# Optimization experiments

Measured on AMD Instinct MI355X. Metric: run time of the kernel, lower is better.

## Reference

```python
import jax, jax.numpy as jnp
import numpy as np


def _ccl(x, w, b):
    # FFT-domain circular conv: rfft2 -> complex multiply + sum over c_in -> irfft2 + bias
    H, W = x.shape[-2], x.shape[-1]
    xf = jnp.fft.rfft2(x)                 # [B, Ci, H, Wf] complex
    wf = jnp.fft.rfft2(w, s=(H, W))       # [Co, Ci, H, Wf] complex
    hf = jnp.einsum('bihw,oihw->bohw', xf, wf)
    return jnp.fft.irfft2(hf, s=(H, W)) + b[:, None, None]


def _maxpool(x, ph, pw):
    B, C, H, W = x.shape
    return x.reshape(B, C, H // ph, ph, W // pw, pw).max(axis=(3, 5))


def _upsample_zero(x, sh, sw):
    B, C, H, W = x.shape
    y = jnp.zeros((B, C, H * sh, W * sw), dtype=x.dtype)
    return y.at[:, :, ::sh, ::sw].set(x)


def setup_inputs() -> dict:
    key = jax.random.key(0)
    ks = jax.random.split(key, 11)
    inp = {"x": jax.random.normal(ks[0], (16, 2, 64, 256), dtype=jnp.float32)}
    specs = [  # (c_out, c_in, kh, kw)
        (50, 1, 3, 7), (50, 50, 3, 7), (50, 50, 3, 5), (50, 50, 3, 7), (1, 50, 3, 7)]
    for i, (co, ci, kh, kw) in enumerate(specs):
        K = float(np.sqrt(1.0 / (ci * kh * kw)))
        inp[f"w{i+1}"] = (2 * jax.random.uniform(ks[2 * i + 1], (co, ci, kh, kw), dtype=jnp.float32) - 1) * K
        inp[f"b{i+1}"] = (2 * jax.random.uniform(ks[2 * i + 2], (co,), dtype=jnp.float32) - 1) * K
    return inp


def reference(x, w1, b1, w2, b2, w3, b3, w4, b4, w5, b5):
    H, W = x.shape[-2], x.shape[-1]
    h = x.reshape(-1, 1, H, W)                       # [2B, 1, 64, 256]
    h = jax.nn.relu(_maxpool(_ccl(h, w1, b1), 2, 4))  # [2B, 50, 32, 64]
    h = jax.nn.relu(_maxpool(_ccl(h, w2, b2), 2, 4))  # [2B, 50, 16, 16]
    h = h.reshape(-1, 2, h.shape[-3], h.shape[-2], h.shape[-1])
    h = h[:, 0] + h[:, 1].mean(axis=(-1, -2))[..., None, None]  # [B, 50, 16, 16]
    h = jax.nn.relu(_ccl(_upsample_zero(h, 2, 4), w3, b3))       # [B, 50, 32, 64]
    h = jax.nn.relu(_ccl(_upsample_zero(h, 2, 4), w4, b4))       # [B, 50, 64, 256]
    h = jax.nn.sigmoid(_ccl(h, w5, b5))                          # [B, 1, 64, 256]
    return h.squeeze(1)
```

## Files before the change

### kernel.cpp

```cpp
#include <hip/hip_runtime.h>
#include <math.h>

__global__ void kprep(const float* __restrict__ w2, const float* __restrict__ w3,
                      const float* __restrict__ w4, float* __restrict__ w2t,
                      float* __restrict__ w3t, float* __restrict__ w4t) {
  int i = blockIdx.x * 256 + threadIdx.x;
  if (i < 52500) {
    int co = i % 50, r = i / 50;
    w2t[i] = w2[co * 1050 + r];
    w4t[i] = w4[co * 1050 + r];
  } else {
    int j = i - 52500;
    if (j < 37500) {
      int co = j % 50, r = j / 50;
      w3t[j] = w3[co * 750 + r];
    }
  }
}

__global__ __launch_bounds__(256) void k1(const float* __restrict__ x,
                                          const float* __restrict__ w1,
                                          const float* __restrict__ b1,
                                          float* __restrict__ a1) {
  int b = blockIdx.z;
  int pr0 = blockIdx.x * 4;
  int co0 = blockIdx.y * 10;
  int ty = threadIdx.x >> 6;
  int pc = threadIdx.x & 63;
  int pr = pr0 + ty;
  const float* xb = x + b * (64 * 256);
  float xw[4][10];
#pragma unroll
  for (int r = 0; r < 4; ++r) {
    int row = (2 * pr - 2 + r) & 63;
#pragma unroll
    for (int c = 0; c < 10; ++c) {
      int col = (4 * pc - 6 + c) & 255;
      xw[r][c] = xb[row * 256 + col];
    }
  }
#pragma unroll
  for (int cq = 0; cq < 10; ++cq) {
    int co = co0 + cq;
    const float* wp = w1 + co * 21;
    float m = -1e30f;
#pragma unroll
    for (int iy = 0; iy < 2; ++iy) {
#pragma unroll
      for (int jx = 0; jx < 4; ++jx) {
        float s = 0.f;
#pragma unroll
        for (int di = 0; di < 3; ++di)
#pragma unroll
          for (int dj = 0; dj < 7; ++dj)
            s = fmaf(xw[iy + 2 - di][jx + 6 - dj], wp[di * 7 + dj], s);
        m = fmaxf(m, s);
      }
    }
    float v = fmaxf(m + b1[co], 0.f);
    a1[((b * 50 + co) * 32 + pr) * 64 + pc] = v;
  }
}

__global__ __launch_bounds__(256) void k2(const float* __restrict__ a1,
                                          const float* __restrict__ w2t,
                                          const float* __restrict__ b2,
                                          float* __restrict__ a2) {
  __shared__ __align__(16) float sm[3840];
  int b = blockIdx.z;
  int r0 = blockIdx.x * 4;
  int co0 = blockIdx.y * 10;
  int y = threadIdx.x >> 6;
  int xcol = threadIdx.x & 63;
  const float* p[7];
#pragma unroll
  for (int dj = 0; dj < 7; ++dj) p[dj] = sm + y * 64 + ((xcol - dj) & 63);
  float acc[10];
#pragma unroll
  for (int co = 0; co < 10; ++co) acc[co] = b2[co0 + co];
  const float* ain = a1 + b * (50 * 2048);
  for (int cci = 0; cci < 5; ++cci) {
    __syncthreads();
    for (int e = threadIdx.x; e < 960; e += 256) {
      int ci = e / 96;
      int rem = e - ci * 96;
      int rr = rem >> 4;
      int c4 = rem & 15;
      int row = (r0 - 2 + rr) & 31;
      *(float4*)&sm[(ci * 6 + rr) * 64 + c4 * 4] =
          *(const float4*)&ain[(cci * 10 + ci) * 2048 + row * 64 + c4 * 4];
    }
    __syncthreads();
    const float* q0 = p[0]; const float* q1 = p[1]; const float* q2 = p[2];
    const float* q3 = p[3]; const float* q4 = p[4]; const float* q5 = p[5];
    const float* q6 = p[6];
    for (int ci = 0; ci < 10; ++ci) {
      const float* wci = w2t + (cci * 10 + ci) * 1050 + co0;
#pragma unroll
      for (int di = 0; di < 3; ++di) {
        const int ro = (2 - di) * 64;
        float xv0 = q0[ro], xv1 = q1[ro], xv2 = q2[ro], xv3 = q3[ro];
        float xv4 = q4[ro], xv5 = q5[ro], xv6 = q6[ro];
        const float* wr = wci + di * 7 * 50;
#pragma unroll
        for (int co = 0; co < 10; ++co) acc[co] = fmaf(xv0, wr[co], acc[co]);
#pragma unroll
        for (int co = 0; co < 10; ++co) acc[co] = fmaf(xv1, wr[50 + co], acc[co]);
#pragma unroll
        for (int co = 0; co < 10; ++co) acc[co] = fmaf(xv2, wr[100 + co], acc[co]);
#pragma unroll
        for (int co = 0; co < 10; ++co) acc[co] = fmaf(xv3, wr[150 + co], acc[co]);
#pragma unroll
        for (int co = 0; co < 10; ++co) acc[co] = fmaf(xv4, wr[200 + co], acc[co]);
#pragma unroll
        for (int co = 0; co < 10; ++co) acc[co] = fmaf(xv5, wr[250 + co], acc[co]);
#pragma unroll
        for (int co = 0; co < 10; ++co) acc[co] = fmaf(xv6, wr[300 + co], acc[co]);
      }
      q0 += 384; q1 += 384; q2 += 384; q3 += 384; q4 += 384; q5 += 384; q6 += 384;
    }
  }
  __syncthreads();
#pragma unroll
  for (int k = 0; k < 10; ++k)
    sm[k * 256 + y * 64 + xcol] = acc[k];
  __syncthreads();
  for (int w = threadIdx.x; w < 320; w += 256) {
    int cop = w / 32;
    int pr = (w >> 4) & 1;
    int pc = w & 15;
    float m = -1e30f;
#pragma unroll
    for (int yy = 0; yy < 2; ++yy)
#pragma unroll
      for (int xx = 0; xx < 4; ++xx)
        m = fmaxf(m, sm[cop * 256 + (pr * 2 + yy) * 64 + pc * 4 + xx]);
    m = fmaxf(m, 0.f);
    a2[((b * 50 + co0 + cop) * 16 + (r0 >> 1) + pr) * 16 + pc] = m;
  }
}

__global__ __launch_bounds__(512) void k3(const float* __restrict__ a2,
                                          const float* __restrict__ w3t,
                                          const float* __restrict__ b3,
                                          float* __restrict__ a3) {
  __shared__ float ts[4000];
  __shared__ float mean_s[64];
  __shared__ float part[200];
  int b = blockIdx.z;
  int r0 = blockIdx.x * 8;
  int co0 = blockIdx.y * 10;
  int tid = threadIdx.x;
  const float* aodd = a2 + (2 * b + 1) * (50 * 256);
  if (tid < 200) {
    int ci = tid >> 2, p = tid & 3;
    float s = 0.f;
    for (int k = 0; k < 64; ++k) s += aodd[ci * 256 + p * 64 + k];
    part[tid] = s;
  }
  __syncthreads();
  if (tid < 50)
    mean_s[tid] = (part[4 * tid] + part[4 * tid + 1] + part[4 * tid + 2] + part[4 * tid + 3]) * (1.f / 256.f);
  __syncthreads();
  const float* aev = a2 + (2 * b) * (50 * 256);
  for (int e = tid; e < 4000; e += 512) {
    int ci = e / 80;
    int rr = (e >> 4) % 5;
    int tc = e & 15;
    int trow = ((r0 >> 1) - 1 + rr) & 15;
    ts[e] = aev[ci * 256 + trow * 16 + tc] + mean_s[ci];
  }
  __syncthreads();
  int wv = __builtin_amdgcn_readfirstlane(tid >> 6);
  int lane = tid & 63;
  int p = wv >> 2;
  int m = wv & 3;
  int q = lane & 15;
  int yidx = lane >> 4;
  int i = r0 + 2 * yidx + p;
  int j = 4 * q + m;
  float acc[10];
#pragma unroll
  for (int co = 0; co < 10; ++co) acc[co] = b3[co0 + co];
  int ndi = (p == 0) ? 2 : 1;
  int ndj = (m == 0) ? 2 : 1;
  for (int aa = 0; aa < ndi; ++aa) {
    int di = (p == 0) ? (2 * aa) : 1;
    int rr = 1 + ((2 * yidx + p - di) >> 1);
    for (int e2 = 0; e2 < ndj; ++e2) {
      int dj = (m == 0) ? (4 * e2) : m;
      int tc = ((j - dj + 64) >> 2) & 15;
      for (int ci = 0; ci < 50; ++ci) {
        float xv = ts[ci * 80 + rr * 16 + tc];
        const float* wrow = w3t + (ci * 15 + di * 5 + dj) * 50 + co0;
#pragma unroll
        for (int co = 0; co < 10; ++co)
          acc[co] = fmaf(xv, wrow[co], acc[co]);
      }
    }
  }
  float* aout = a3 + b * (50 * 2048);
#pragma unroll
  for (int co = 0; co < 10; ++co)
    aout[(co0 + co) * 2048 + i * 64 + j] = fmaxf(acc[co], 0.f);
}

__global__ __launch_bounds__(512) void k4(const float* __restrict__ a3,
                                          const float* __restrict__ w4t,
                                          const float* __restrict__ b4,
                                          float* __restrict__ a4) {
  __shared__ float s4[6400];
  int b = blockIdx.z;
  int r0 = blockIdx.x * 2;
  int co0 = blockIdx.y * 10;
  int tid = threadIdx.x;
  const float* ain = a3 + b * (50 * 2048);
  for (int e = tid; e < 6400; e += 512) {
    int ci = e >> 7;
    int rr = (e >> 6) & 1;
    int col = e & 63;
    int row = ((r0 >> 1) - 1 + rr) & 31;
    s4[e] = ain[ci * 2048 + row * 64 + col];
  }
  __syncthreads();
  int wv = __builtin_amdgcn_readfirstlane(tid >> 6);
  int lane = tid & 63;
  int rowsel = wv >> 2;
  int m = wv & 3;
  int i = r0 + rowsel;
  int j = 4 * lane + m;
  float acc[10];
#pragma unroll
  for (int co = 0; co < 10; ++co) acc[co] = b4[co0 + co];
  int ndi = (rowsel == 0) ? 2 : 1;
  int ndj = (m < 3) ? 2 : 1;
  for (int aa = 0; aa < ndi; ++aa) {
    int di = (rowsel == 0) ? (2 * aa) : 1;
    int rr = 1 - (di >> 1);
    for (int e2 = 0; e2 < ndj; ++e2) {
      int dj = m + 4 * e2;
      int tc = ((j - dj) >> 2) & 63;
      for (int ci = 0; ci < 50; ++ci) {
        float xv = s4[ci * 128 + rr * 64 + tc];
        const float* wrow = w4t + (ci * 21 + di * 7 + dj) * 50 + co0;
#pragma unroll
        for (int co = 0; co < 10; ++co)
          acc[co] = fmaf(xv, wrow[co], acc[co]);
      }
    }
  }
  float* aout = a4 + b * (50 * 16384);
#pragma unroll
  for (int co = 0; co < 10; ++co)
    aout[(co0 + co) * 16384 + i * 256 + j] = fmaxf(acc[co], 0.f);
}

__global__ __launch_bounds__(256) void k5(const float* __restrict__ a4,
                                          const float* __restrict__ w5,
                                          const float* __restrict__ b5,
                                          float* __restrict__ out) {
  __shared__ float s5[2400];
  __shared__ float smw5[1056];
  int bid = blockIdx.x;
  int b = bid >> 6;
  int rem = bid & 63;
  int r0 = (rem >> 2) * 4;
  int jb = (rem & 3) * 64;
  int tid = threadIdx.x;
  int y = tid >> 6;
  int q = tid & 63;
  for (int e = tid; e < 1050; e += 256) smw5[e] = w5[e];
  float acc = b5[0];
  const float* ain = a4 + b * (50 * 16384);
  for (int cc = 0; cc < 10; ++cc) {
    __syncthreads();
    for (int e = tid; e < 2400; e += 256) {
      int ci = e / 480;
      int rr = (e / 80) % 6;
      int c = e % 80;
      int row = (r0 - 2 + rr) & 63;
      int col = (jb + c - 8) & 255;
      s5[e] = ain[(cc * 5 + ci) * 16384 + row * 256 + col];
    }
    __syncthreads();
#pragma unroll
    for (int ci = 0; ci < 5; ++ci) {
#pragma unroll
      for (int di = 0; di < 3; ++di) {
        const float* base = s5 + ci * 480 + (y + 2 - di) * 80 + 8 + q;
        const float* wp = smw5 + ((cc * 5 + ci) * 3 + di) * 7;
#pragma unroll
        for (int dj = 0; dj < 7; ++dj)
          acc = fmaf(base[-dj], wp[dj], acc);
      }
    }
  }
  out[b * 16384 + (r0 + y) * 256 + jb + q] = 1.f / (1.f + expf(-acc));
}

extern "C" void kernel_launch(void* const* d_in, const int* in_sizes, int n_in,
                              void* d_out, int out_size, void* d_ws, size_t ws_size,
                              hipStream_t stream) {
  (void)in_sizes; (void)n_in; (void)out_size; (void)ws_size;
  const float* x  = (const float*)d_in[0];
  const float* w1 = (const float*)d_in[1];
  const float* b1 = (const float*)d_in[2];
  const float* w2 = (const float*)d_in[3];
  const float* b2 = (const float*)d_in[4];
  const float* w3 = (const float*)d_in[5];
  const float* b3 = (const float*)d_in[6];
  const float* w4 = (const float*)d_in[7];
  const float* b4 = (const float*)d_in[8];
  const float* w5 = (const float*)d_in[9];
  const float* b5 = (const float*)d_in[10];
  float* out = (float*)d_out;
  float* ws  = (float*)d_ws;
  float* w2t = ws;
  float* w3t = w2t + 52500;
  float* w4t = w3t + 37500;
  float* a1  = w4t + 52500;
  float* a2  = a1 + 32 * 50 * 32 * 64;
  float* a3  = a2 + 32 * 50 * 16 * 16;
  float* a4  = a3 + 16 * 50 * 32 * 64;
  hipLaunchKernelGGL(kprep, dim3(352), dim3(256), 0, stream, w2, w3, w4, w2t, w3t, w4t);
  hipLaunchKernelGGL(k1, dim3(8, 5, 32), dim3(256), 0, stream, x, w1, b1, a1);
  hipLaunchKernelGGL(k2, dim3(8, 5, 32), dim3(256), 0, stream, a1, w2t, b2, a2);
  hipLaunchKernelGGL(k3, dim3(4, 5, 16), dim3(512), 0, stream, a2, w3t, b3, a3);
  hipLaunchKernelGGL(k4, dim3(32, 5, 16), dim3(512), 0, stream, a3, w4t, b4, a4);
  hipLaunchKernelGGL(k5, dim3(1024), dim3(256), 0, stream, a4, w5, b5, out);
}
```

Baseline: 340.7 us.

## Fold weight transpose into k1, register-block k4 over two rows, widen k5 tiles

The separate weight-transpose kernel is removed and its work is appended to the k1 blocks with blockIdx.y==0, saving one launch. k4 now computes two output rows per thread (rows i and i+2) so each weight load is reused twice, and it stages its input with float4 loads over a three-row halo. k5 now uses 512-thread blocks covering 8 rows with float4 staging, which cuts redundant halo loads. In exchange, register pressure in k4 rises, the grids get fewer blocks, and there is a tail of transpose work inside k1.

```diff
diff --git a/kernel.cpp b/kernel.cpp
--- a/kernel.cpp
+++ b/kernel.cpp
@@ -1,27 +1,16 @@
 #include <hip/hip_runtime.h>
 #include <math.h>
-
-__global__ void kprep(const float* __restrict__ w2, const float* __restrict__ w3,
-                      const float* __restrict__ w4, float* __restrict__ w2t,
-                      float* __restrict__ w3t, float* __restrict__ w4t) {
-  int i = blockIdx.x * 256 + threadIdx.x;
-  if (i < 52500) {
-    int co = i % 50, r = i / 50;
-    w2t[i] = w2[co * 1050 + r];
-    w4t[i] = w4[co * 1050 + r];
-  } else {
-    int j = i - 52500;
-    if (j < 37500) {
-      int co = j % 50, r = j / 50;
-      w3t[j] = w3[co * 750 + r];
-    }
-  }
-}
 
 __global__ __launch_bounds__(256) void k1(const float* __restrict__ x,
                                           const float* __restrict__ w1,
                                           const float* __restrict__ b1,
-                                          float* __restrict__ a1) {
+                                          float* __restrict__ a1,
+                                          const float* __restrict__ w2,
+                                          const float* __restrict__ w3,
+                                          const float* __restrict__ w4,
+                                          float* __restrict__ w2t,
+                                          float* __restrict__ w3t,
+                                          float* __restrict__ w4t) {
   int b = blockIdx.z;
   int pr0 = blockIdx.x * 4;
   int co0 = blockIdx.y * 10;
@@ -59,6 +48,20 @@
     }
     float v = fmaxf(m + b1[co], 0.f);
     a1[((b * 50 + co) * 32 + pr) * 64 + pc] = v;
+  }
+  if (blockIdx.y == 0) {
+    int base = (blockIdx.z * 8 + blockIdx.x) * 256 + threadIdx.x;
+    for (int i = base; i < 90000; i += 65536) {
+      if (i < 52500) {
+        int co = i % 50, r = i / 50;
+        w2t[i] = w2[co * 1050 + r];
+        w4t[i] = w4[co * 1050 + r];
+      } else {
+        int j2 = i - 52500;
+        int co = j2 % 50, r = j2 / 50;
+        w3t[j2] = w3[co * 750 + r];
+      }
+    }
   }
 }
 
@@ -209,85 +212,99 @@
                                           const float* __restrict__ w4t,
                                           const float* __restrict__ b4,
                                           float* __restrict__ a4) {
-  __shared__ float s4[6400];
+  __shared__ __align__(16) float s4[9600];
   int b = blockIdx.z;
-  int r0 = blockIdx.x * 2;
+  int r0 = blockIdx.x * 4;
   int co0 = blockIdx.y * 10;
   int tid = threadIdx.x;
   const float* ain = a3 + b * (50 * 2048);
-  for (int e = tid; e < 6400; e += 512) {
-    int ci = e >> 7;
-    int rr = (e >> 6) & 1;
-    int col = e & 63;
-    int row = ((r0 >> 1) - 1 + rr) & 31;
-    s4[e] = ain[ci * 2048 + row * 64 + col];
+  int prb = (r0 >> 1) - 1;
+  for (int e = tid; e < 2400; e += 512) {
+    int ci = e / 48;
+    int rem = e - ci * 48;
+    int rr = rem >> 4;
+    int c4 = rem & 15;
+    int row = (prb + rr) & 31;
+    *(float4*)&s4[(ci * 3 + rr) * 64 + c4 * 4] =
+        *(const float4*)&ain[ci * 2048 + row * 64 + c4 * 4];
   }
   __syncthreads();
   int wv = __builtin_amdgcn_readfirstlane(tid >> 6);
   int lane = tid & 63;
   int rowsel = wv >> 2;
   int m = wv & 3;
-  int i = r0 + rowsel;
   int j = 4 * lane + m;
-  float acc[10];
-#pragma unroll
-  for (int co = 0; co < 10; ++co) acc[co] = b4[co0 + co];
+  float acc[2][10];
+#pragma unroll
+  for (int co = 0; co < 10; ++co) {
+    float bc = b4[co0 + co];
+    acc[0][co] = bc; acc[1][co] = bc;
+  }
   int ndi = (rowsel == 0) ? 2 : 1;
   int ndj = (m < 3) ? 2 : 1;
   for (int aa = 0; aa < ndi; ++aa) {
     int di = (rowsel == 0) ? (2 * aa) : 1;
-    int rr = 1 - (di >> 1);
+    int rrb = 1 + ((rowsel - di) >> 1);
     for (int e2 = 0; e2 < ndj; ++e2) {
       int dj = m + 4 * e2;
       int tc = ((j - dj) >> 2) & 63;
       for (int ci = 0; ci < 50; ++ci) {
-        float xv = s4[ci * 128 + rr * 64 + tc];
+        float xv0 = s4[ci * 192 + rrb * 64 + tc];
+        float xv1 = s4[ci * 192 + (rrb + 1) * 64 + tc];
         const float* wrow = w4t + (ci * 21 + di * 7 + dj) * 50 + co0;
 #pragma unroll
-        for (int co = 0; co < 10; ++co)
-          acc[co] = fmaf(xv, wrow[co], acc[co]);
+        for (int co = 0; co < 10; ++co) {
+          float w = wrow[co];
+          acc[0][co] = fmaf(xv0, w, acc[0][co]);
+          acc[1][co] = fmaf(xv1, w, acc[1][co]);
+        }
       }
     }
   }
   float* aout = a4 + b * (50 * 16384);
-#pragma unroll
-  for (int co = 0; co < 10; ++co)
-    aout[(co0 + co) * 16384 + i * 256 + j] = fmaxf(acc[co], 0.f);
-}
-
-__global__ __launch_bounds__(256) void k5(const float* __restrict__ a4,
+  int i0 = r0 + rowsel, i1 = r0 + rowsel + 2;
+#pragma unroll
+  for (int co = 0; co < 10; ++co) {
+    aout[(co0 + co) * 16384 + i0 * 256 + j] = fmaxf(acc[0][co], 0.f);
+    aout[(co0 + co) * 16384 + i1 * 256 + j] = fmaxf(acc[1][co], 0.f);
+  }
+}
+
+__global__ __launch_bounds__(512) void k5(const float* __restrict__ a4,
                                           const float* __restrict__ w5,
                                           const float* __restrict__ b5,
                                           float* __restrict__ out) {
-  __shared__ float s5[2400];
+  __shared__ __align__(16) float s5[4000];
   __shared__ float smw5[1056];
   int bid = blockIdx.x;
-  int b = bid >> 6;
-  int rem = bid & 63;
-  int r0 = (rem >> 2) * 4;
+  int b = bid >> 5;
+  int rem = bid & 31;
+  int r0 = (rem >> 2) * 8;
   int jb = (rem & 3) * 64;
   int tid = threadIdx.x;
   int y = tid >> 6;
   int q = tid & 63;
-  for (int e = tid; e < 1050; e += 256) smw5[e] = w5[e];
+  for (int e = tid; e < 1050; e += 512) smw5[e] = w5[e];
   float acc = b5[0];
   const float* ain = a4 + b * (50 * 16384);
   for (int cc = 0; cc < 10; ++cc) {
     __syncthreads();
-    for (int e = tid; e < 2400; e += 256) {
-      int ci = e / 480;
-      int rr = (e / 80) % 6;
-      int c = e % 80;
+    for (int e = tid; e < 1000; e += 512) {
+      int ci = e / 200;
+      int rem2 = e - ci * 200;
+      int rr = rem2 / 20;
+      int g = rem2 - rr * 20;
       int row = (r0 - 2 + rr) & 63;
-      int col = (jb + c - 8) & 255;
-      s5[e] = ain[(cc * 5 + ci) * 16384 + row * 256 + col];
+      int col = (jb + 4 * g - 8) & 255;
+      *(float4*)&s5[(ci * 10 + rr) * 80 + 4 * g] =
+          *(const float4*)&ain[(cc * 5 + ci) * 16384 + row * 256 + col];
     }
     __syncthreads();
 #pragma unroll
     for (int ci = 0; ci < 5; ++ci) {
 #pragma unroll
       for (int di = 0; di < 3; ++di) {
-        const float* base = s5 + ci * 480 + (y + 2 - di) * 80 + 8 + q;
+        const float* base = s5 + ci * 800 + (y + 2 - di) * 80 + 8 + q;
         const float* wp = smw5 + ((cc * 5 + ci) * 3 + di) * 7;
 #pragma unroll
         for (int dj = 0; dj < 7; ++dj)
@@ -322,10 +339,10 @@
   float* a2  = a1 + 32 * 50 * 32 * 64;
   float* a3  = a2 + 32 * 50 * 16 * 16;
   float* a4  = a3 + 16 * 50 * 32 * 64;
-  hipLaunchKernelGGL(kprep, dim3(352), dim3(256), 0, stream, w2, w3, w4, w2t, w3t, w4t);
-  hipLaunchKernelGGL(k1, dim3(8, 5, 32), dim3(256), 0, stream, x, w1, b1, a1);
+  hipLaunchKernelGGL(k1, dim3(8, 5, 32), dim3(256), 0, stream, x, w1, b1, a1,
+                     w2, w3, w4, w2t, w3t, w4t);
   hipLaunchKernelGGL(k2, dim3(8, 5, 32), dim3(256), 0, stream, a1, w2t, b2, a2);
   hipLaunchKernelGGL(k3, dim3(4, 5, 16), dim3(512), 0, stream, a2, w3t, b3, a3);
-  hipLaunchKernelGGL(k4, dim3(32, 5, 16), dim3(512), 0, stream, a3, w4t, b4, a4);
-  hipLaunchKernelGGL(k5, dim3(1024), dim3(256), 0, stream, a4, w5, b5, out);
-}
+  hipLaunchKernelGGL(k4, dim3(16, 5, 16), dim3(512), 0, stream, a3, w4t, b4, a4);
+  hipLaunchKernelGGL(k5, dim3(512), dim3(512), 0, stream, a4, w5, b5, out);
+}
```

Result: faster. 313.3 us (-8.1%).
